# Performance work log

Measured on AMD Instinct MI355X. Metric: run time of the kernel, lower is better.

## Reference

```python
import jax, jax.numpy as jnp
import numpy as np

ALPHA = 1.702
LIMIT = 7.0


def setup_inputs() -> dict:
    key = jax.random.key(0)
    ks = jax.random.split(key, 6)
    B, T, H, I, E = 2, 1024, 2048, 2048, 8
    hidden_states = jax.random.normal(ks[0], (B, T, H), dtype=jnp.float32)
    routing_weights = jax.random.uniform(ks[1], (B * T, E), dtype=jnp.float32)
    routing_weights = routing_weights / routing_weights.sum(-1, keepdims=True)
    gate_up_proj = jax.random.normal(ks[2], (E, H, 2 * I), dtype=jnp.float32) * 0.02
    gate_up_proj_bias = jax.random.normal(ks[3], (E, 2 * I), dtype=jnp.float32) * 0.02
    down_proj = jax.random.normal(ks[4], (E, I, H), dtype=jnp.float32) * 0.02
    down_proj_bias = jax.random.normal(ks[5], (E, H), dtype=jnp.float32) * 0.02
    return {
        "hidden_states": hidden_states,
        "routing_weights": routing_weights,
        "gate_up_proj": gate_up_proj,
        "gate_up_proj_bias": gate_up_proj_bias,
        "down_proj": down_proj,
        "down_proj_bias": down_proj_bias,
    }


def reference(hidden_states, routing_weights, gate_up_proj, gate_up_proj_bias,
              down_proj, down_proj_bias):
    # Inference branch of GptOssExperts: dense repeat-all-experts grouped GEMM
    B, T, H = hidden_states.shape
    x = hidden_states.reshape(-1, H)                      # [N, H]
    # [E, N, 2I]
    gate_up = jnp.einsum('nh,ehd->end', x, gate_up_proj) + gate_up_proj_bias[:, None, :]
    gate = gate_up[..., ::2]                              # interleaved split
    up = gate_up[..., 1::2]
    gate = jnp.minimum(gate, LIMIT)
    up = jnp.clip(up, -LIMIT, LIMIT)
    glu = gate * jax.nn.sigmoid(gate * ALPHA)
    # [E, N, H]
    out = jnp.einsum('eni,eih->enh', (up + 1.0) * glu, down_proj) + down_proj_bias[:, None, :]
    out = out * routing_weights.T[..., None]              # weight per (expert, token)
    return out.sum(axis=0).reshape(B, T, H)
```

## Files before the change

kernel.cpp:

```cpp
#include <hip/hip_runtime.h>
#include <cstdint>
#include <cstddef>

#define ALPHA 1.702f
#define LIMIT 7.0f

#define NTOK 2048
#define HDIM 2048
#define IDIM 2048
#define I2   4096
#define NEXP 8

typedef float f32x4 __attribute__((ext_vector_type(4)));
typedef short bf16x8 __attribute__((ext_vector_type(8)));
typedef unsigned short u16;

__device__ __forceinline__ u16 f2bf(float f) {
  unsigned u = __float_as_uint(f);
  u += 0x7fffu + ((u >> 16) & 1u);
  return (u16)(u >> 16);
}

__device__ __forceinline__ void gload_lds16(const void* g, void* l) {
  __builtin_amdgcn_global_load_lds(
      (const __attribute__((address_space(1))) void*)g,
      (__attribute__((address_space(3))) void*)l, 16, 0, 0);
}

#define BARRIER() do { asm volatile("" ::: "memory"); __builtin_amdgcn_s_barrier(); asm volatile("" ::: "memory"); } while (0)
#define VMCNT(n)  asm volatile("s_waitcnt vmcnt(" #n ")" ::: "memory")

__global__ __launch_bounds__(256) void k_cvt(const float* __restrict__ in,
                                             u16* __restrict__ out) {
  int i = blockIdx.x * blockDim.x + threadIdx.x;
  const float4* p = (const float4*)in + (size_t)i * 2;
  float4 a = p[0], b = p[1];
  union { u16 s[8]; uint4 v; } o;
  o.s[0] = f2bf(a.x); o.s[1] = f2bf(a.y); o.s[2] = f2bf(a.z); o.s[3] = f2bf(a.w);
  o.s[4] = f2bf(b.x); o.s[5] = f2bf(b.y); o.s[6] = f2bf(b.z); o.s[7] = f2bf(b.w);
  ((uint4*)out)[i] = o.v;
}

__global__ __launch_bounds__(256) void k_tc(const float* __restrict__ in,
                                            u16* __restrict__ out, int R, int C) {
  __shared__ float tile[32][33];
  const size_t mo = (size_t)blockIdx.z * R * C;
  const float* ip = in + mo;
  u16* op = out + mo;
  int c0 = blockIdx.x * 32, r0 = blockIdx.y * 32;
  int t = threadIdx.x;
  int tr = t >> 3, tc = (t & 7) * 4;
  float4 v = *(const float4*)&ip[(size_t)(r0 + tr) * C + c0 + tc];
  tile[tr][tc] = v.x; tile[tr][tc + 1] = v.y;
  tile[tr][tc + 2] = v.z; tile[tr][tc + 3] = v.w;
  __syncthreads();
  ushort4 o;
  o.x = f2bf(tile[tc + 0][tr]);
  o.y = f2bf(tile[tc + 1][tr]);
  o.z = f2bf(tile[tc + 2][tr]);
  o.w = f2bf(tile[tc + 3][tr]);
  *(ushort4*)&op[(size_t)(c0 + tr) * R + r0 + tc] = o;
}

#define MFMA_Q(mh, nh, bb) \
  _Pragma("unroll") for (int mm = 0; mm < 4; ++mm) \
  _Pragma("unroll") for (int nn = 0; nn < 2; ++nn) \
  _Pragma("unroll") for (int ks = 0; ks < 2; ++ks) \
    acc[(mh)*4+mm][(nh)*2+nn] = __builtin_amdgcn_mfma_f32_16x16x32_bf16( \
        a[mm][ks], (bb)[nn][ks], acc[(mh)*4+mm][(nh)*2+nn], 0, 0, 0);

__global__ __launch_bounds__(512, 2) void k_gemm1(const u16* __restrict__ xbf,
                                                  const u16* __restrict__ w1t,
                                                  const float* __restrict__ gub,
                                                  const float* __restrict__ rw,
                                                  u16* __restrict__ inter) {
  __shared__ __align__(16) u16 Als[4][128 * 64];
  __shared__ __align__(16) u16 Bls[4][128 * 64];

  const int bid = (int)blockIdx.x;
  const int L = (bid & 7) * 128 + (bid >> 3);
  const int mtile = L & 7, ntile = (L >> 3) & 15, e = L >> 7;
  const int row0 = mtile * 256, col0 = ntile * 256;
  const u16* A = xbf;
  const u16* B = w1t + (size_t)e * I2 * HDIM;

  const int tid = threadIdx.x;
  const int w = tid >> 6, lane = tid & 63;
  const int wr = w >> 2, wc = w & 3;
  const int rrow = lane & 15, klane = lane >> 4;
  const int sA = (wr * 64 + rrow) * 64;
  const int sB = (wc * 32 + rrow) * 64;
  int kofs[2];
  kofs[0] = ((klane ^ (rrow & 7)) << 3);
  kofs[1] = (((4 + klane) ^ (rrow & 7)) << 3);

  auto stA = [&](int reg, int h, int k0) {
#pragma unroll
    for (int j = 0; j < 2; ++j) {
      int c = (w * 2 + j) * 64 + lane;
      int r = c >> 3, gg = c & 7;
      int ksw = ((gg ^ (r & 7)) << 3);
      int R = ((r >> 6) << 7) + h * 64 + (r & 63);
      gload_lds16(A + (size_t)(row0 + R) * HDIM + k0 + ksw,
                  &Als[reg][(size_t)(w * 2 + j) * 512]);
    }
  };
  auto stB = [&](int reg, int h, int k0) {
#pragma unroll
    for (int j = 0; j < 2; ++j) {
      int c = (w * 2 + j) * 64 + lane;
      int r = c >> 3, gg = c & 7;
      int ksw = ((gg ^ (r & 7)) << 3);
      int C = ((r >> 5) << 6) + h * 32 + (r & 31);
      gload_lds16(B + (size_t)(col0 + C) * HDIM + k0 + ksw,
                  &Bls[reg][(size_t)(w * 2 + j) * 512]);
    }
  };

  f32x4 acc[8][4];
#pragma unroll
  for (int i = 0; i < 8; ++i)
#pragma unroll
    for (int j = 0; j < 4; ++j) acc[i][j] = (f32x4){0.f, 0.f, 0.f, 0.f};

  bf16x8 a[4][2], b0[2][2], b1[2][2];
  auto rdA = [&](int reg) {
#pragma unroll
    for (int mm = 0; mm < 4; ++mm)
#pragma unroll
      for (int ks = 0; ks < 2; ++ks)
        a[mm][ks] = *(const bf16x8*)&Als[reg][sA + mm * 1024 + kofs[ks]];
  };
  auto rdB0 = [&](int reg) {
#pragma unroll
    for (int nn = 0; nn < 2; ++nn)
#pragma unroll
      for (int ks = 0; ks < 2; ++ks)
        b0[nn][ks] = *(const bf16x8*)&Bls[reg][sB + nn * 1024 + kofs[ks]];
  };
  auto rdB1 = [&](int reg) {
#pragma unroll
    for (int nn = 0; nn < 2; ++nn)
#pragma unroll
      for (int ks = 0; ks < 2; ++ks)
        b1[nn][ks] = *(const bf16x8*)&Bls[reg][sB + nn * 1024 + kofs[ks]];
  };

  stB(0, 0, 0); stB(1, 1, 0); stA(0, 0, 0); stA(1, 1, 0);
  stB(2, 0, 64); stB(3, 1, 64); stA(2, 0, 64);
  VMCNT(8);
  BARRIER();

  for (int i = 0; i < 16; ++i) {
    const int t = 2 * i;
    const int kA1 = (t + 1) * 64;
    const int kN0 = (t + 2 < 32 ? t + 2 : 31) * 64;
    const int kN1 = (t + 3 < 32 ? t + 3 : 31) * 64;

    rdA(0); rdB0(0);
    stA(3, 1, kA1);
    BARRIER();
    __builtin_amdgcn_s_setprio(1); MFMA_Q(0, 0, b0); __builtin_amdgcn_s_setprio(0);
    BARRIER();

    rdB1(1);
    stB(0, 0, kN0);
    BARRIER();
    __builtin_amdgcn_s_setprio(1); MFMA_Q(0, 1, b1); __builtin_amdgcn_s_setprio(0);
    VMCNT(10);
    BARRIER();

    rdA(1);
    stB(1, 1, kN0);
    BARRIER();
    __builtin_amdgcn_s_setprio(1); MFMA_Q(1, 0, b0); __builtin_amdgcn_s_setprio(0);
    BARRIER();

    stA(0, 0, kN0);
    BARRIER();
    __builtin_amdgcn_s_setprio(1); MFMA_Q(1, 1, b1); __builtin_amdgcn_s_setprio(0);
    VMCNT(8);
    BARRIER();

    rdA(2); rdB0(2);
    stA(1, 1, kN0);
    BARRIER();
    __builtin_amdgcn_s_setprio(1); MFMA_Q(0, 0, b0); __builtin_amdgcn_s_setprio(0);
    BARRIER();

    rdB1(3);
    stB(2, 0, kN1);
    BARRIER();
    __builtin_amdgcn_s_setprio(1); MFMA_Q(0, 1, b1); __builtin_amdgcn_s_setprio(0);
    VMCNT(10);
    BARRIER();

    rdA(3);
    stB(3, 1, kN1);
    BARRIER();
    __builtin_amdgcn_s_setprio(1); MFMA_Q(1, 0, b0); __builtin_amdgcn_s_setprio(0);
    BARRIER();

    stA(2, 0, kN1);
    BARRIER();
    __builtin_amdgcn_s_setprio(1); MFMA_Q(1, 1, b1); __builtin_amdgcn_s_setprio(0);
    VMCNT(8);
    BARRIER();
  }

  const float* bias = gub + (size_t)e * I2;
  u16* ip = inter + (size_t)e * NTOK * IDIM;
#pragma unroll
  for (int ai = 0; ai < 8; ++ai) {
    const int mh = ai >> 2, mm = ai & 3;
#pragma unroll
    for (int bj = 0; bj < 4; ++bj) {
      const int nh = bj >> 1, nn = bj & 1;
      const int col = col0 + wc * 64 + nh * 32 + nn * 16 + rrow;
      const float bv = bias[col];
#pragma unroll
      for (int r = 0; r < 4; ++r) {
        const int row = row0 + wr * 128 + mh * 64 + mm * 16 + klane * 4 + r;
        float gu = acc[ai][bj][r] + bv;
        float pg = __shfl_xor(gu, 1);
        float gate = (lane & 1) ? pg : gu;
        float up   = (lane & 1) ? gu : pg;
        gate = fminf(gate, LIMIT);
        up = fminf(fmaxf(up, -LIMIT), LIMIT);
        float glu = gate / (1.f + __expf(-ALPHA * gate));
        float val = (up + 1.f) * glu * rw[row * NEXP + e];
        if (!(lane & 1)) ip[(size_t)row * IDIM + (col >> 1)] = f2bf(val);
      }
    }
  }
}

__global__ __launch_bounds__(512, 2) void k_gemm2(const u16* __restrict__ inter,
                                                  const u16* __restrict__ w2t,
                                                  float* __restrict__ part) {
  __shared__ __align__(16) u16 Als[4][128 * 64];
  __shared__ __align__(16) u16 Bls[4][128 * 64];

  const int bid = (int)blockIdx.x;
  const int L = (bid & 7) * 32 + (bid >> 3);
  const int mtile = L & 7, ntile = (L >> 3) & 7, sp = L >> 6;
  const int row0 = mtile * 256, col0 = ntile * 256;
  const int es = sp * 2;

  const int tid = threadIdx.x;
  const int w = tid >> 6, lane = tid & 63;
  const int wr = w >> 2, wc = w & 3;
  const int rrow = lane & 15, klane = lane >> 4;
  const int sA = (wr * 64 + rrow) * 64;
  const int sB = (wc * 32 + rrow) * 64;
  int kofs[2];
  kofs[0] = ((klane ^ (rrow & 7)) << 3);
  kofs[1] = (((4 + klane) ^ (rrow & 7)) << 3);

  auto stA = [&](int reg, int h, int k0) {
    const u16* Ab = inter + (size_t)(es + (k0 >> 11)) * NTOK * IDIM;
    const int kk = k0 & 2047;
#pragma unroll
    for (int j = 0; j < 2; ++j) {
      int c = (w * 2 + j) * 64 + lane;
      int r = c >> 3, gg = c & 7;
      int ksw = ((gg ^ (r & 7)) << 3);
      int R = ((r >> 6) << 7) + h * 64 + (r & 63);
      gload_lds16(Ab + (size_t)(row0 + R) * IDIM + kk + ksw,
                  &Als[reg][(size_t)(w * 2 + j) * 512]);
    }
  };
  auto stB = [&](int reg, int h, int k0) {
    const u16* Bb = w2t + (size_t)(es + (k0 >> 11)) * HDIM * IDIM;
    const int kk = k0 & 2047;
#pragma unroll
    for (int j = 0; j < 2; ++j) {
      int c = (w * 2 + j) * 64 + lane;
      int r = c >> 3, gg = c & 7;
      int ksw = ((gg ^ (r & 7)) << 3);
      int C = ((r >> 5) << 6) + h * 32 + (r & 31);
      gload_lds16(Bb + (size_t)(col0 + C) * IDIM + kk + ksw,
                  &Bls[reg][(size_t)(w * 2 + j) * 512]);
    }
  };

  f32x4 acc[8][4];
#pragma unroll
  for (int i = 0; i < 8; ++i)
#pragma unroll
    for (int j = 0; j < 4; ++j) acc[i][j] = (f32x4){0.f, 0.f, 0.f, 0.f};

  bf16x8 a[4][2], b0[2][2], b1[2][2];
  auto rdA = [&](int reg) {
#pragma unroll
    for (int mm = 0; mm < 4; ++mm)
#pragma unroll
      for (int ks = 0; ks < 2; ++ks)
        a[mm][ks] = *(const bf16x8*)&Als[reg][sA + mm * 1024 + kofs[ks]];
  };
  auto rdB0 = [&](int reg) {
#pragma unroll
    for (int nn = 0; nn < 2; ++nn)
#pragma unroll
      for (int ks = 0; ks < 2; ++ks)
        b0[nn][ks] = *(const bf16x8*)&Bls[reg][sB + nn * 1024 + kofs[ks]];
  };
  auto rdB1 = [&](int reg) {
#pragma unroll
    for (int nn = 0; nn < 2; ++nn)
#pragma unroll
      for (int ks = 0; ks < 2; ++ks)
        b1[nn][ks] = *(const bf16x8*)&Bls[reg][sB + nn * 1024 + kofs[ks]];
  };

  stB(0, 0, 0); stB(1, 1, 0); stA(0, 0, 0); stA(1, 1, 0);
  stB(2, 0, 64); stB(3, 1, 64); stA(2, 0, 64);
  VMCNT(8);
  BARRIER();

  for (int i = 0; i < 32; ++i) {
    const int t = 2 * i;
    const int kA1 = (t + 1) * 64;
    const int kN0 = (t + 2 < 64 ? t + 2 : 63) * 64;
    const int kN1 = (t + 3 < 64 ? t + 3 : 63) * 64;

    rdA(0); rdB0(0);
    stA(3, 1, kA1);
    BARRIER();
    __builtin_amdgcn_s_setprio(1); MFMA_Q(0, 0, b0); __builtin_amdgcn_s_setprio(0);
    BARRIER();

    rdB1(1);
    stB(0, 0, kN0);
    BARRIER();
    __builtin_amdgcn_s_setprio(1); MFMA_Q(0, 1, b1); __builtin_amdgcn_s_setprio(0);
    VMCNT(10);
    BARRIER();

    rdA(1);
    stB(1, 1, kN0);
    BARRIER();
    __builtin_amdgcn_s_setprio(1); MFMA_Q(1, 0, b0); __builtin_amdgcn_s_setprio(0);
    BARRIER();

    stA(0, 0, kN0);
    BARRIER();
    __builtin_amdgcn_s_setprio(1); MFMA_Q(1, 1, b1); __builtin_amdgcn_s_setprio(0);
    VMCNT(8);
    BARRIER();

    rdA(2); rdB0(2);
    stA(1, 1, kN0);
    BARRIER();
    __builtin_amdgcn_s_setprio(1); MFMA_Q(0, 0, b0); __builtin_amdgcn_s_setprio(0);
    BARRIER();

    rdB1(3);
    stB(2, 0, kN1);
    BARRIER();
    __builtin_amdgcn_s_setprio(1); MFMA_Q(0, 1, b1); __builtin_amdgcn_s_setprio(0);
    VMCNT(10);
    BARRIER();

    rdA(3);
    stB(3, 1, kN1);
    BARRIER();
    __builtin_amdgcn_s_setprio(1); MFMA_Q(1, 0, b0); __builtin_amdgcn_s_setprio(0);
    BARRIER();

    stA(2, 0, kN1);
    BARRIER();
    __builtin_amdgcn_s_setprio(1); MFMA_Q(1, 1, b1); __builtin_amdgcn_s_setprio(0);
    VMCNT(8);
    BARRIER();
  }

  float* pp = part + (size_t)sp * NTOK * HDIM;
#pragma unroll
  for (int ai = 0; ai < 8; ++ai) {
    const int mh = ai >> 2, mm = ai & 3;
#pragma unroll
    for (int bj = 0; bj < 4; ++bj) {
      const int nh = bj >> 1, nn = bj & 1;
      const int col = col0 + wc * 64 + nh * 32 + nn * 16 + rrow;
#pragma unroll
      for (int r = 0; r < 4; ++r) {
        const int row = row0 + wr * 128 + mh * 64 + mm * 16 + klane * 4 + r;
        pp[(size_t)row * HDIM + col] = acc[ai][bj][r];
      }
    }
  }
}

__global__ __launch_bounds__(256) void k_reduce(const float* __restrict__ part,
                                                const float* __restrict__ dbias,
                                                const float* __restrict__ rw,
                                                float* __restrict__ out) {
  const int i = blockIdx.x * 256 + threadIdx.x;
  const int i4 = i * 4;
  const int n = i4 >> 11;
  const int h = i4 & 2047;
  const size_t MSZ = (size_t)NTOK * HDIM / 4;
  const float4* p = (const float4*)part;
  float4 v0 = p[i];
  float4 v1 = p[i + MSZ];
  float4 v2 = p[i + 2 * MSZ];
  float4 v3 = p[i + 3 * MSZ];
  float4 s;
  s.x = (v0.x + v1.x) + (v2.x + v3.x);
  s.y = (v0.y + v1.y) + (v2.y + v3.y);
  s.z = (v0.z + v1.z) + (v2.z + v3.z);
  s.w = (v0.w + v1.w) + (v2.w + v3.w);
#pragma unroll
  for (int e = 0; e < NEXP; ++e) {
    float rwe = rw[n * NEXP + e];
    float4 db = *(const float4*)&dbias[(size_t)e * HDIM + h];
    s.x += rwe * db.x; s.y += rwe * db.y;
    s.z += rwe * db.z; s.w += rwe * db.w;
  }
  *(float4*)&out[i4] = s;
}

extern "C" void kernel_launch(void* const* d_in, const int* in_sizes, int n_in,
                              void* d_out, int out_size, void* d_ws, size_t ws_size,
                              hipStream_t stream) {
  const float* hs   = (const float*)d_in[0];
  const float* rw   = (const float*)d_in[1];
  const float* gup  = (const float*)d_in[2];
  const float* gupb = (const float*)d_in[3];
  const float* dwn  = (const float*)d_in[4];
  const float* dwnb = (const float*)d_in[5];
  float* out = (float*)d_out;

  u16* xbf   = (u16*)d_ws;
  u16* w1t   = xbf + (size_t)NTOK * HDIM;
  u16* w2t   = w1t + (size_t)NEXP * I2 * HDIM;
  u16* inter = w2t + (size_t)NEXP * HDIM * IDIM;
  float* part = (float*)w1t;
  size_t need = ((size_t)NTOK * HDIM + (size_t)NEXP * I2 * HDIM +
                 (size_t)NEXP * HDIM * IDIM + (size_t)NEXP * NTOK * IDIM) * 2;
  if (ws_size < need) return;

  k_cvt<<<(NTOK * HDIM) / (256 * 8), 256, 0, stream>>>(hs, xbf);

  dim3 g1(I2 / 32, HDIM / 32, NEXP);
  k_tc<<<g1, 256, 0, stream>>>(gup, w1t, HDIM, I2);
  dim3 g2(HDIM / 32, IDIM / 32, NEXP);
  k_tc<<<g2, 256, 0, stream>>>(dwn, w2t, IDIM, HDIM);

  k_gemm1<<<dim3(1024), 512, 0, stream>>>(xbf, w1t, gupb, rw, inter);

  k_gemm2<<<dim3(256), 512, 0, stream>>>(inter, w2t, part);

  k_reduce<<<dim3(NTOK * HDIM / 1024), 256, 0, stream>>>(part, dwnb, rw, out);
}
```

Before: 563.3 us.

## Restructure GEMM main loops into two-phase schedule with fewer barriers

Both grouped-GEMM main loops are rewritten from an 8-phase, 2-tile-unrolled schedule into a 2-phase per-K-tile schedule. Each phase now issues two MFMA quadrants between barriers instead of one, and the global-to-LDS loads for the next tile are grouped together. The vmcnt waits are adjusted to match. The aim is to halve barrier count and give larger MFMA bursts that hide LDS and global latency better. In exchange, more fragments are live at once and load/compute interleaving is coarser, which could hurt overlap or register pressure.

```diff
diff --git a/kernel.cpp b/kernel.cpp
--- a/kernel.cpp
+++ b/kernel.cpp
@@ -148,63 +148,30 @@
 
   stB(0, 0, 0); stB(1, 1, 0); stA(0, 0, 0); stA(1, 1, 0);
   stB(2, 0, 64); stB(3, 1, 64); stA(2, 0, 64);
-  VMCNT(8);
+  VMCNT(6);
   BARRIER();
 
-  for (int i = 0; i < 16; ++i) {
-    const int t = 2 * i;
-    const int kA1 = (t + 1) * 64;
-    const int kN0 = (t + 2 < 32 ? t + 2 : 31) * 64;
-    const int kN1 = (t + 3 < 32 ? t + 3 : 31) * 64;
-
-    rdA(0); rdB0(0);
-    stA(3, 1, kA1);
-    BARRIER();
-    __builtin_amdgcn_s_setprio(1); MFMA_Q(0, 0, b0); __builtin_amdgcn_s_setprio(0);
-    BARRIER();
-
-    rdB1(1);
-    stB(0, 0, kN0);
-    BARRIER();
-    __builtin_amdgcn_s_setprio(1); MFMA_Q(0, 1, b1); __builtin_amdgcn_s_setprio(0);
-    VMCNT(10);
-    BARRIER();
-
-    rdA(1);
-    stB(1, 1, kN0);
-    BARRIER();
-    __builtin_amdgcn_s_setprio(1); MFMA_Q(1, 0, b0); __builtin_amdgcn_s_setprio(0);
-    BARRIER();
-
-    stA(0, 0, kN0);
-    BARRIER();
-    __builtin_amdgcn_s_setprio(1); MFMA_Q(1, 1, b1); __builtin_amdgcn_s_setprio(0);
-    VMCNT(8);
-    BARRIER();
-
-    rdA(2); rdB0(2);
-    stA(1, 1, kN0);
-    BARRIER();
-    __builtin_amdgcn_s_setprio(1); MFMA_Q(0, 0, b0); __builtin_amdgcn_s_setprio(0);
-    BARRIER();
-
-    rdB1(3);
-    stB(2, 0, kN1);
-    BARRIER();
-    __builtin_amdgcn_s_setprio(1); MFMA_Q(0, 1, b1); __builtin_amdgcn_s_setprio(0);
-    VMCNT(10);
-    BARRIER();
-
-    rdA(3);
-    stB(3, 1, kN1);
-    BARRIER();
-    __builtin_amdgcn_s_setprio(1); MFMA_Q(1, 0, b0); __builtin_amdgcn_s_setprio(0);
-    BARRIER();
-
-    stA(2, 0, kN1);
-    BARRIER();
-    __builtin_amdgcn_s_setprio(1); MFMA_Q(1, 1, b1); __builtin_amdgcn_s_setprio(0);
-    VMCNT(8);
+  for (int t = 0; t < 32; ++t) {
+    const int b = t & 1;
+    const int kA1 = (t + 1 < 32 ? t + 1 : 31) * 64;
+    const int kN  = (t + 2 < 32 ? t + 2 : 31) * 64;
+    const int rA1 = 2 * ((t + 1) & 1) + 1;
+
+    rdA(2 * b); rdB0(2 * b); rdB1(2 * b + 1);
+    stA(rA1, 1, kA1);
+    BARRIER();
+    __builtin_amdgcn_s_setprio(1);
+    MFMA_Q(0, 0, b0); MFMA_Q(0, 1, b1);
+    __builtin_amdgcn_s_setprio(0);
+    BARRIER();
+
+    rdA(2 * b + 1);
+    stB(2 * b, 0, kN); stB(2 * b + 1, 1, kN); stA(2 * b, 0, kN);
+    BARRIER();
+    __builtin_amdgcn_s_setprio(1);
+    MFMA_Q(1, 0, b0); MFMA_Q(1, 1, b1);
+    __builtin_amdgcn_s_setprio(0);
+    VMCNT(6);
     BARRIER();
   }
 
@@ -315,63 +282,30 @@
 
   stB(0, 0, 0); stB(1, 1, 0); stA(0, 0, 0); stA(1, 1, 0);
   stB(2, 0, 64); stB(3, 1, 64); stA(2, 0, 64);
-  VMCNT(8);
+  VMCNT(6);
   BARRIER();
 
-  for (int i = 0; i < 32; ++i) {
-    const int t = 2 * i;
-    const int kA1 = (t + 1) * 64;
-    const int kN0 = (t + 2 < 64 ? t + 2 : 63) * 64;
-    const int kN1 = (t + 3 < 64 ? t + 3 : 63) * 64;
-
-    rdA(0); rdB0(0);
-    stA(3, 1, kA1);
-    BARRIER();
-    __builtin_amdgcn_s_setprio(1); MFMA_Q(0, 0, b0); __builtin_amdgcn_s_setprio(0);
-    BARRIER();
-
-    rdB1(1);
-    stB(0, 0, kN0);
-    BARRIER();
-    __builtin_amdgcn_s_setprio(1); MFMA_Q(0, 1, b1); __builtin_amdgcn_s_setprio(0);
-    VMCNT(10);
-    BARRIER();
-
-    rdA(1);
-    stB(1, 1, kN0);
-    BARRIER();
-    __builtin_amdgcn_s_setprio(1); MFMA_Q(1, 0, b0); __builtin_amdgcn_s_setprio(0);
-    BARRIER();
-
-    stA(0, 0, kN0);
-    BARRIER();
-    __builtin_amdgcn_s_setprio(1); MFMA_Q(1, 1, b1); __builtin_amdgcn_s_setprio(0);
-    VMCNT(8);
-    BARRIER();
-
-    rdA(2); rdB0(2);
-    stA(1, 1, kN0);
-    BARRIER();
-    __builtin_amdgcn_s_setprio(1); MFMA_Q(0, 0, b0); __builtin_amdgcn_s_setprio(0);
-    BARRIER();
-
-    rdB1(3);
-    stB(2, 0, kN1);
-    BARRIER();
-    __builtin_amdgcn_s_setprio(1); MFMA_Q(0, 1, b1); __builtin_amdgcn_s_setprio(0);
-    VMCNT(10);
-    BARRIER();
-
-    rdA(3);
-    stB(3, 1, kN1);
-    BARRIER();
-    __builtin_amdgcn_s_setprio(1); MFMA_Q(1, 0, b0); __builtin_amdgcn_s_setprio(0);
-    BARRIER();
-
-    stA(2, 0, kN1);
-    BARRIER();
-    __builtin_amdgcn_s_setprio(1); MFMA_Q(1, 1, b1); __builtin_amdgcn_s_setprio(0);
-    VMCNT(8);
+  for (int t = 0; t < 64; ++t) {
+    const int b = t & 1;
+    const int kA1 = (t + 1 < 64 ? t + 1 : 63) * 64;
+    const int kN  = (t + 2 < 64 ? t + 2 : 63) * 64;
+    const int rA1 = 2 * ((t + 1) & 1) + 1;
+
+    rdA(2 * b); rdB0(2 * b); rdB1(2 * b + 1);
+    stA(rA1, 1, kA1);
+    BARRIER();
+    __builtin_amdgcn_s_setprio(1);
+    MFMA_Q(0, 0, b0); MFMA_Q(0, 1, b1);
+    __builtin_amdgcn_s_setprio(0);
+    BARRIER();
+
+    rdA(2 * b + 1);
+    stB(2 * b, 0, kN); stB(2 * b + 1, 1, kN); stA(2 * b, 0, kN);
+    BARRIER();
+    __builtin_amdgcn_s_setprio(1);
+    MFMA_Q(1, 0, b0); MFMA_Q(1, 1, b1);
+    __builtin_amdgcn_s_setprio(0);
+    VMCNT(6);
     BARRIER();
   }
 
```

Result: slower. 591.5 us (+5.0%).
